# Kernel optimization log

Measured on AMD Instinct MI355X. Metric: run time of the kernel, lower is better.

Reference implementation:

```python
import jax, jax.numpy as jnp
import numpy as np

N_EMBD = 1024
N_HEAD = 16


def setup_inputs() -> dict:
    key = jax.random.key(0)
    ks = jax.random.split(key, 11)
    B, T, T2, C = 4, 2048, 1024, N_EMBD
    s = 0.02
    return {
        "x": jax.random.normal(ks[0], (B, T, C), jnp.float32),
        "enc_x": jax.random.normal(ks[1], (B, T2, C), jnp.float32),
        "Wq": jax.random.normal(ks[2], (C, C), jnp.float32) * s,
        "bq": jax.random.normal(ks[3], (C,), jnp.float32) * s,
        "Wk": jax.random.normal(ks[4], (C, C), jnp.float32) * s,
        "bk": jax.random.normal(ks[5], (C,), jnp.float32) * s,
        "Wv": jax.random.normal(ks[6], (C, C), jnp.float32) * s,
        "bv": jax.random.normal(ks[7], (C,), jnp.float32) * s,
        "Wo": jax.random.normal(ks[8], (C, C), jnp.float32) * s,
        "bo": jax.random.normal(ks[9], (C,), jnp.float32) * s,
    }


def reference(x, enc_x, Wq, bq, Wk, bk, Wv, bv, Wo, bo):
    B, T, C = x.shape
    B2, T2, C2 = enc_x.shape
    H = N_HEAD
    D = C // H  # head dim
    q = x @ Wq + bq          # [B,T,C]
    k = enc_x @ Wk + bk      # [B,T2,C]
    v = enc_x @ Wv + bv      # [B,T2,C]
    q = q.reshape(B, T, H, D).transpose(0, 2, 1, 3)    # [B,H,T,D]
    k = k.reshape(B2, T2, H, D).transpose(0, 2, 1, 3)  # [B,H,T2,D]
    v = v.reshape(B2, T2, H, D).transpose(0, 2, 1, 3)  # [B,H,T2,D]
    att = jnp.einsum("bhtd,bhsd->bhts", q, k) * (1.0 / jnp.sqrt(jnp.float32(D)))
    att = jax.nn.softmax(att, axis=-1)                 # [B,H,T,T2]
    y = jnp.einsum("bhts,bhsd->bhtd", att, v)          # [B,H,T,D]
    y = y.transpose(0, 2, 1, 3).reshape(B, T, C)
    return y @ Wo + bo
```

## Files before the change

### kernel.cpp

```cpp
#include <hip/hip_runtime.h>
#include <hip/hip_bf16.h>


typedef __bf16 bf16_t;
typedef __bf16 bf16x8 __attribute__((ext_vector_type(8)));
typedef float f32x4 __attribute__((ext_vector_type(4)));
typedef float f32x16 __attribute__((ext_vector_type(16)));
typedef unsigned int u32x4 __attribute__((ext_vector_type(4)));

#define AS1C(p) ((const __attribute__((address_space(1))) void*)(p))
#define AS3(p)  ((__attribute__((address_space(3))) void*)(p))

constexpr int CC  = 1024;
constexpr int TT  = 2048;
constexpr int TT2 = 1024;

#if __has_builtin(__builtin_amdgcn_exp2f)
__device__ __forceinline__ float EXP2(float x) { return __builtin_amdgcn_exp2f(x); }
#else
__device__ __forceinline__ float EXP2(float x) { return exp2f(x); }
#endif

__global__ __launch_bounds__(256) void prep(const float* __restrict__ x, bf16_t* __restrict__ xb,
                                            const float* __restrict__ enc, bf16_t* __restrict__ eb,
                                            const float* __restrict__ W0, const float* __restrict__ W1,
                                            const float* __restrict__ W2, const float* __restrict__ W3,
                                            bf16_t* __restrict__ T0, bf16_t* __restrict__ T1,
                                            bf16_t* __restrict__ T2, bf16_t* __restrict__ T3) {
    __shared__ float tile[32][33];
    const int bid = blockIdx.x;
    if (bid < 2048) {
        int t = bid * 256 + threadIdx.x;
        #pragma unroll
        for (int k = 0; k < 3; ++k) {
            int i = t + k * 524288;
            const float* in; bf16_t* out; int j;
            if (i < 1048576) { in = x;   out = xb; j = i; }
            else             { in = enc; out = eb; j = i - 1048576; }
            const float4* p = (const float4*)in + 2 * (size_t)j;
            float4 a = p[0], b = p[1];
            bf16x8 v;
            v[0] = (bf16_t)a.x; v[1] = (bf16_t)a.y; v[2] = (bf16_t)a.z; v[3] = (bf16_t)a.w;
            v[4] = (bf16_t)b.x; v[5] = (bf16_t)b.y; v[6] = (bf16_t)b.z; v[7] = (bf16_t)b.w;
            *(bf16x8*)(out + (size_t)j * 8) = v;
        }
    } else {
        int idx = bid - 2048;
        int bx = idx & 31, by = (idx >> 5) & 31, bz = idx >> 10;
        const float* W; bf16_t* Tt;
        switch (bz) {
            case 0:  W = W0; Tt = T0; break;
            case 1:  W = W1; Tt = T1; break;
            case 2:  W = W2; Tt = T2; break;
            default: W = W3; Tt = T3; break;
        }
        int xx = threadIdx.x & 31, yy = threadIdx.x >> 5;
        int bxe = bx * 32, bye = by * 32;
        for (int i = 0; i < 4; ++i) {
            int r = yy + i * 8;
            tile[r][xx] = W[(size_t)(bye + r) * 1024 + bxe + xx];
        }
        __syncthreads();
        for (int i = 0; i < 4; ++i) {
            int r = yy + i * 8;
            Tt[(size_t)(bxe + r) * 1024 + bye + xx] = (bf16_t)tile[xx][r];
        }
    }
}

#define SB0 __builtin_amdgcn_sched_barrier(0)
#define GLL(src, dst) __builtin_amdgcn_global_load_lds(AS1C(src), AS3(dst), 16, 0, 0)

__device__ __forceinline__ bf16x8 ldx(const char* p) { return *(const bf16x8*)p; }

__global__ __launch_bounds__(512, 2) void gemm_qkv8(const bf16_t* __restrict__ xb,
                                                    const bf16_t* __restrict__ eb,
                                                    const bf16_t* __restrict__ wtq,
                                                    const bf16_t* __restrict__ wtk,
                                                    const float* __restrict__ bq,
                                                    const float* __restrict__ bk,
                                                    const float* __restrict__ bv,
                                                    bf16_t* __restrict__ Qs,
                                                    bf16_t* __restrict__ Ks,
                                                    bf16_t* __restrict__ Vs,
                                                    float qscale) {
    __shared__ __align__(16) char GLDS[131072];
    char* ldsA = &GLDS[0];
    char* ldsB = &GLDS[65536];

    const int tid = threadIdx.x;
    const int w   = tid >> 6;
    const int l   = tid & 63;
    const int wm  = w >> 2;
    const int wn  = w & 3;
    const int l15 = l & 15, lhi = l >> 4;

    const int bid = blockIdx.x;
    const bf16_t* Ap; const bf16_t* Bp;
    int m0, n0;
    float scale;
    const float* bias; bf16_t* outp; int outn0;
    bool vout = false;
    if (bid < 128) {
        int xcd = bid & 7, j = bid >> 3;
        n0 = (j & 3) * 256; m0 = (xcd * 4 + (j >> 2)) * 256;
        Ap = xb; Bp = wtq; scale = qscale;
        bias = bq; outp = Qs; outn0 = n0;
    } else {
        int b2 = bid - 128;
        int xcd = b2 & 7, j = b2 >> 3;
        n0 = (j & 7) * 256; m0 = (xcd * 2 + (j >> 3)) * 256;
        Ap = eb; Bp = wtk; scale = 1.0f;
        if (n0 < 1024) { bias = bk; outp = Ks; outn0 = n0; }
        else           { bias = bv; outp = Vs; outn0 = n0 - 1024; vout = true; }
    }

    const int lrow  = l >> 3;
    const int lslot = (l & 7) ^ lrow;
    const char* Asrc = (const char*)(Ap + (size_t)(m0 + w * 16 + lrow) * 1024 + lslot * 8);
    const char* Bsrc = (const char*)(Bp + (size_t)(n0 + w * 16 + lrow) * 1024 + lslot * 8);
    #define STG_A(t, buf, h)                                                                   \
        do {                                                                                   \
            GLL(Asrc + (size_t)(h) * 262144 + (t) * 128,         ldsA + (buf) * 32768 + (h) * 16384 + w * 2048);        \
            GLL(Asrc + (size_t)(h) * 262144 + 16384 + (t) * 128, ldsA + (buf) * 32768 + (h) * 16384 + w * 2048 + 1024); \
        } while (0)
    #define STG_B(t, buf, h)                                                                   \
        do {                                                                                   \
            GLL(Bsrc + (size_t)(h) * 262144 + (t) * 128,         ldsB + (buf) * 32768 + (h) * 16384 + w * 2048);        \
            GLL(Bsrc + (size_t)(h) * 262144 + 16384 + (t) * 128, ldsB + (buf) * 32768 + (h) * 16384 + w * 2048 + 1024); \
        } while (0)

    const int aoff = (wm * 128 + l15) * 128;
    const int boff = (wn * 64 + l15) * 128;
    const int sl0  = ((0 + lhi) ^ (l15 & 7)) << 4;
    const int sl1  = ((4 + lhi) ^ (l15 & 7)) << 4;

    #define RD_A(dst, KA, qm)                                                    \
        do { _Pragma("unroll") for (int mf = 0; mf < 4; ++mf) {                  \
            dst[mf * 2 + 0] = ldx((KA) + aoff + ((qm) * 64 + mf * 16) * 128 + sl0); \
            dst[mf * 2 + 1] = ldx((KA) + aoff + ((qm) * 64 + mf * 16) * 128 + sl1); } } while (0)
    #define RD_B(dst, KB, qn)                                                    \
        do { _Pragma("unroll") for (int nf = 0; nf < 2; ++nf) {                  \
            dst[nf * 2 + 0] = ldx((KB) + boff + ((qn) * 32 + nf * 16) * 128 + sl0); \
            dst[nf * 2 + 1] = ldx((KB) + boff + ((qn) * 32 + nf * 16) * 128 + sl1); } } while (0)

    #define MFMA16(qm, qn, Af, Bf)                                                             \
        do { __builtin_amdgcn_s_setprio(1);                                                    \
            _Pragma("unroll") for (int mf = 0; mf < 4; ++mf)                                   \
            _Pragma("unroll") for (int nf = 0; nf < 2; ++nf) {                                 \
                acc[(qm) * 4 + mf][(qn) * 2 + nf] = __builtin_amdgcn_mfma_f32_16x16x32_bf16(   \
                    Af[mf * 2 + 0], Bf[nf * 2 + 0], acc[(qm) * 4 + mf][(qn) * 2 + nf], 0, 0, 0); \
                acc[(qm) * 4 + mf][(qn) * 2 + nf] = __builtin_amdgcn_mfma_f32_16x16x32_bf16(   \
                    Af[mf * 2 + 1], Bf[nf * 2 + 1], acc[(qm) * 4 + mf][(qn) * 2 + nf], 0, 0, 0); } \
            __builtin_amdgcn_s_setprio(0); } while (0)

    #define PH_BAR do { SB0; __builtin_amdgcn_s_barrier(); SB0;                                \
                        asm volatile("s_waitcnt lgkmcnt(0)" ::: "memory"); SB0; } while (0)
    #define PH_END do { SB0; __builtin_amdgcn_s_barrier(); SB0; } while (0)

    f32x4 acc[8][4] = {};
    bf16x8 A0[8], A1[8], B0[4], B1[4];

    STG_A(0, 0, 0); STG_A(0, 0, 1);
    STG_B(0, 0, 0); STG_B(0, 0, 1);
    STG_A(1, 1, 0); STG_A(1, 1, 1);
    asm volatile("s_waitcnt vmcnt(4)" ::: "memory");
    SB0; __builtin_amdgcn_s_barrier(); SB0;

    constexpr int NT = 16;
    for (int t = 0; t < NT; ++t) {
        const int buf = t & 1;
        const char* KA = ldsA + buf * 32768;
        const char* KB = ldsB + buf * 32768;

        if (t + 1 < NT) STG_B(t + 1, buf ^ 1, 0);
        RD_A(A0, KA, 0); RD_B(B0, KB, 0);
        PH_BAR;
        MFMA16(0, 0, A0, B0);
        PH_END;

        if (t + 1 < NT) STG_B(t + 1, buf ^ 1, 1);
        RD_A(A1, KA, 1);
        PH_BAR;
        MFMA16(1, 0, A1, B0);
        PH_END;

        if (t + 2 < NT) STG_A(t + 2, buf, 0);
        RD_B(B1, KB, 1);
        PH_BAR;
        MFMA16(1, 1, A1, B1);
        PH_END;

        if (t + 2 < NT) STG_A(t + 2, buf, 1);
        SB0; __builtin_amdgcn_s_barrier(); SB0;
        MFMA16(0, 1, A0, B1);
        if (t < NT - 2) asm volatile("s_waitcnt vmcnt(4)" ::: "memory");
        else            asm volatile("s_waitcnt vmcnt(0)" ::: "memory");
        PH_END;
    }

    __syncthreads();
    char* EP = GLDS + w * 16384;

    if (!vout) {
        #pragma unroll
        for (int ni = 0; ni < 4; ++ni) {
            int c_rel = ni * 16 + l15;
            float bvv = bias[outn0 + wn * 64 + c_rel];
            #pragma unroll
            for (int mi = 0; mi < 8; ++mi) {
                int mbase = mi * 16 + lhi * 4;
                #pragma unroll
                for (int r = 0; r < 4; ++r)
                    *(bf16_t*)(EP + (mbase + r) * 128 + c_rel * 2) =
                        (bf16_t)((acc[mi][ni][r] + bvv) * scale);
            }
        }
        asm volatile("s_waitcnt lgkmcnt(0)" ::: "memory");
        SB0;
        char* gbase = (char*)outp + (size_t)(m0 + wm * 128) * 2048 + (outn0 + wn * 64) * 2;
        #pragma unroll
        for (int i = 0; i < 16; ++i) {
            int m_rel = i * 8 + (l >> 3);
            int ch = l & 7;
            bf16x8 v = *(const bf16x8*)(EP + m_rel * 128 + ch * 16);
            *(bf16x8*)(gbase + (size_t)m_rel * 2048 + ch * 16) = v;
        }
    } else {
        int col0 = outn0 + wn * 64;
        int hh = col0 >> 6;
        int rowbase = m0 + wm * 128;
        int bb = rowbase >> 10, key0 = rowbase & 1023;
        #pragma unroll
        for (int ni = 0; ni < 4; ++ni) {
            int dd = ni * 16 + l15;
            float bvv = bias[col0 + dd];
            int sw = (dd & 7) << 4;
            #pragma unroll
            for (int mi = 0; mi < 8; ++mi) {
                int kb = mi * 16 + lhi * 4;
                #pragma unroll
                for (int r = 0; r < 4; ++r)
                    *(bf16_t*)(EP + dd * 256 + (((kb + r) * 2) ^ sw)) =
                        (bf16_t)((acc[mi][ni][r] + bvv) * scale);
            }
        }
        asm volatile("s_waitcnt lgkmcnt(0)" ::: "memory");
        SB0;
        char* gbase = (char*)outp + ((size_t)((bb * 16 + hh) * 64) * 1024 + key0) * 2;
        #pragma unroll
        for (int i = 0; i < 16; ++i) {
            int dd = i * 4 + (l >> 4);
            int ch = l & 15;
            bf16x8 v = *(const bf16x8*)(EP + dd * 256 + ((ch * 16) ^ ((dd & 7) << 4)));
            *(bf16x8*)(gbase + (size_t)dd * 2048 + ch * 16) = v;
        }
    }
    #undef STG_A
    #undef STG_B
    #undef RD_A
    #undef RD_B
    #undef MFMA16
    #undef PH_BAR
    #undef PH_END
}

__device__ __forceinline__ void gemm_body(bf16_t* As, bf16_t* Bs,
                                          const bf16_t* __restrict__ A,
                                          const bf16_t* __restrict__ Bt,
                                          const float* __restrict__ bias,
                                          float* __restrict__ out,
                                          int lgNT, int mband, int bid) {
    const int tid  = threadIdx.x;
    const int lane = tid & 63;
    const int wave = tid >> 6;
    const int wr = wave >> 1, wc = wave & 1;
    const int l15 = lane & 15, lhi = lane >> 4;

    const int xcd = bid & 7;
    const int j   = bid >> 3;
    const int n0  = (j & ((1 << lgNT) - 1)) * 128;
    const int m0  = (xcd * mband + (j >> lgNT)) * 128;

    f32x4 acc[4][4] = {};

    for (int k0 = 0; k0 < 1024; k0 += 32) {
        for (int i = 0; i < 2; ++i) {
            int e   = i * 2048 + wave * 512 + lane * 8;
            int row = e >> 5, col = e & 31;
            __builtin_amdgcn_global_load_lds(AS1C(A  + (size_t)(m0 + row) * 1024 + k0 + col),
                                             AS3(As + i * 2048 + wave * 512), 16, 0, 0);
            __builtin_amdgcn_global_load_lds(AS1C(Bt + (size_t)(n0 + row) * 1024 + k0 + col),
                                             AS3(Bs + i * 2048 + wave * 512), 16, 0, 0);
        }
        __syncthreads();
        bf16x8 a[4], b[4];
        #pragma unroll
        for (int m = 0; m < 4; ++m)
            a[m] = *(const bf16x8*)&As[(wr * 64 + m * 16 + l15) * 32 + lhi * 8];
        #pragma unroll
        for (int n = 0; n < 4; ++n)
            b[n] = *(const bf16x8*)&Bs[(wc * 64 + n * 16 + l15) * 32 + lhi * 8];
        #pragma unroll
        for (int m = 0; m < 4; ++m)
            #pragma unroll
            for (int n = 0; n < 4; ++n)
                acc[m][n] = __builtin_amdgcn_mfma_f32_16x16x32_bf16(a[m], b[n], acc[m][n], 0, 0, 0);
        __syncthreads();
    }

    #pragma unroll
    for (int n = 0; n < 4; ++n) {
        int col = n0 + wc * 64 + n * 16 + l15;
        float bv = bias[col];
        #pragma unroll
        for (int m = 0; m < 4; ++m) {
            int rowb = m0 + wr * 64 + m * 16 + lhi * 4;
            #pragma unroll
            for (int r = 0; r < 4; ++r)
                out[(size_t)(rowb + r) * 1024 + col] = acc[m][n][r] + bv;
        }
    }
}

__global__ __launch_bounds__(256) void gemm_out(const bf16_t* __restrict__ yb,
                                                const bf16_t* __restrict__ wto,
                                                const float* __restrict__ bo,
                                                float* __restrict__ out) {
    __shared__ __align__(16) bf16_t As[128 * 32];
    __shared__ __align__(16) bf16_t Bs[128 * 32];
    gemm_body(As, Bs, yb, wto, bo, out, 3, 8, blockIdx.x);
}

__device__ __forceinline__ unsigned pk_bf16(float lo, float hi) {
    unsigned r;
    asm("v_cvt_pk_bf16_f32 %0, %1, %2" : "=v"(r) : "v"(lo), "v"(hi));
    return r;
}
__device__ __forceinline__ void swap32(unsigned &a, unsigned &b) {
    asm("v_permlane32_swap_b32 %0, %1" : "+v"(a), "+v"(b));
}
__device__ __forceinline__ float sum_halves(float x) {
    unsigned a = __builtin_bit_cast(unsigned, x), b = a;
    swap32(a, b);
    return __builtin_bit_cast(float, a) + __builtin_bit_cast(float, b);
}
__device__ __forceinline__ bf16x8 ldsf(const bf16_t* base, int row, int colb) {
    int off = row * 128 + (colb ^ ((row & 7) << 4));
    return *(const bf16x8*)((const char*)base + off);
}
__device__ __forceinline__ bf16x8 packP(const f32x16& s0, const f32x16& s1, int kt) {
    const f32x16& sp = (kt < 2) ? s0 : s1;
    const int rb = (kt & 1) * 8;
    unsigned a0 = pk_bf16(sp[rb + 0], sp[rb + 1]);
    unsigned a1 = pk_bf16(sp[rb + 2], sp[rb + 3]);
    unsigned a2 = pk_bf16(sp[rb + 4], sp[rb + 5]);
    unsigned a3 = pk_bf16(sp[rb + 6], sp[rb + 7]);
    swap32(a0, a2);
    swap32(a1, a3);
    union { u32x4 u; bf16x8 h; } cv;
    cv.u = (u32x4){a0, a1, a2, a3};
    return cv.h;
}

__global__ __launch_bounds__(256, 2) void attn256(const bf16_t* __restrict__ Q,
                                                  const bf16_t* __restrict__ K,
                                                  const bf16_t* __restrict__ Vt,
                                                  bf16_t* __restrict__ Y) {
    __shared__ __align__(16) bf16_t SM[3][2][64 * 64];

    const int tid = threadIdx.x;
    const int l   = tid & 63;
    const int w   = tid >> 6;
    const int l31 = l & 31;
    const int lh  = l >> 5;

    const int bid = blockIdx.x;
    const int bh  = bid & 63;
    const int qb  = bid >> 6;
    const int b = bh >> 4, h = bh & 15;
    const int q0 = qb * 256 + w * 64;

    const bf16_t* Qb = Q + (size_t)b * TT * CC + h * 64;
    const char* Kc = (const char*)(K + (size_t)b * TT2 * CC + h * 64);
    const char* Vc = (const char*)(Vt + (size_t)bh * 64 * 1024);

    bf16x8 qfA[4], qfB[4];
    #pragma unroll
    for (int kt = 0; kt < 4; ++kt) {
        qfA[kt] = *(const bf16x8*)&Qb[(size_t)(q0 + l31)      * CC + kt * 16 + lh * 8];
        qfB[kt] = *(const bf16x8*)&Qb[(size_t)(q0 + 32 + l31) * CC + kt * 16 + lh * 8];
    }
    __builtin_amdgcn_sched_barrier(0);

    f32x16 yA0 = {}, yA1 = {}, yB0 = {}, yB1 = {};
    float lsA = 0.f, lsB = 0.f;

    const int krow = w * 16 + (l >> 3);
    const int ss   = ((l & 7) ^ (l >> 3)) & 7;
    const int off0 = krow * 2048 + ss * 16;
    const int off1 = off0 + 8 * 2048;

    #define STAGE(t, buf)                                                                 \
        do {                                                                              \
            __builtin_amdgcn_global_load_lds(AS1C(Kc + (size_t)(t) * 131072 + off0),      \
                                             AS3((char*)&SM[buf][0][0] + w * 2048), 16, 0, 0);        \
            __builtin_amdgcn_global_load_lds(AS1C(Kc + (size_t)(t) * 131072 + off1),      \
                                             AS3((char*)&SM[buf][0][0] + w * 2048 + 1024), 16, 0, 0); \
            __builtin_amdgcn_global_load_lds(AS1C(Vc + (t) * 128 + off0),                 \
                                             AS3((char*)&SM[buf][1][0] + w * 2048), 16, 0, 0);        \
            __builtin_amdgcn_global_load_lds(AS1C(Vc + (t) * 128 + off1),                 \
                                             AS3((char*)&SM[buf][1][0] + w * 2048 + 1024), 16, 0, 0); \
        } while (0)

    #define SUMEXP(s0, s1, ls)                                                    \
        do {                                                                      \
            float rs = 0.f;                                                       \
            _Pragma("unroll")                                                     \
            for (int r = 0; r < 16; ++r) {                                        \
                s0[r] = EXP2(s0[r]);                                              \
                s1[r] = EXP2(s1[r]);                                              \
                rs += s0[r] + s1[r];                                              \
            }                                                                     \
            ls += sum_halves(rs);                                                 \
        } while (0)

    constexpr int NT = TT2 / 64;
    STAGE(0, 0);
    STAGE(1, 1);

    int cur = 0;
    for (int t = 0; t < NT; ++t) {
        if (t + 1 < NT) asm volatile("s_waitcnt vmcnt(4)" ::: "memory");
        else            asm volatile("s_waitcnt vmcnt(0)" ::: "memory");
        __builtin_amdgcn_sched_barrier(0);
        __builtin_amdgcn_s_barrier();
        __builtin_amdgcn_sched_barrier(0);

        if (t + 2 < NT) {
            int nb = cur + 2; if (nb >= 3) nb -= 3;
            STAGE(t + 2, nb);
        }

        const bf16_t* Kl = &SM[cur][0][0];
        const bf16_t* Vl = &SM[cur][1][0];

        f32x16 sA0 = {}, sA1 = {}, sB0 = {}, sB1 = {};
        #pragma unroll
        for (int kt = 0; kt < 4; ++kt) {
            int colb = kt * 32 + (lh << 4);
            bf16x8 a0 = ldsf(Kl, l31,      colb);
            bf16x8 a1 = ldsf(Kl, 32 + l31, colb);
            sA0 = __builtin_amdgcn_mfma_f32_32x32x16_bf16(a0, qfA[kt], sA0, 0, 0, 0);
            sB0 = __builtin_amdgcn_mfma_f32_32x32x16_bf16(a0, qfB[kt], sB0, 0, 0, 0);
            sA1 = __builtin_amdgcn_mfma_f32_32x32x16_bf16(a1, qfA[kt], sA1, 0, 0, 0);
            sB1 = __builtin_amdgcn_mfma_f32_32x32x16_bf16(a1, qfB[kt], sB1, 0, 0, 0);
        }

        SUMEXP(sA0, sA1, lsA);
        SUMEXP(sB0, sB1, lsB);

        __builtin_amdgcn_s_setprio(1);
        #pragma unroll
        for (int kt = 0; kt < 4; ++kt) {
            bf16x8 pA = packP(sA0, sA1, kt);
            bf16x8 pB = packP(sB0, sB1, kt);
            int colb = kt * 32 + (lh << 4);
            bf16x8 v0 = ldsf(Vl, l31,      colb);
            bf16x8 v1 = ldsf(Vl, 32 + l31, colb);
            yA0 = __builtin_amdgcn_mfma_f32_32x32x16_bf16(v0, pA, yA0, 0, 0, 0);
            yA1 = __builtin_amdgcn_mfma_f32_32x32x16_bf16(v1, pA, yA1, 0, 0, 0);
            yB0 = __builtin_amdgcn_mfma_f32_32x32x16_bf16(v0, pB, yB0, 0, 0, 0);
            yB1 = __builtin_amdgcn_mfma_f32_32x32x16_bf16(v1, pB, yB1, 0, 0, 0);
        }
        __builtin_amdgcn_s_setprio(0);

        ++cur; if (cur == 3) cur = 0;
    }
    #undef STAGE
    #undef SUMEXP

    __syncthreads();

    float iA = 1.f / lsA, iB = 1.f / lsB;
    char* ob = (char*)&SM[0][0][0] + w * 8192;
    const int sw = (l31 & 7) << 4;
    #pragma unroll
    for (int r = 0; r < 16; ++r) {
        int drow = (r & 3) + 8 * (r >> 2) + 4 * lh;
        *(bf16_t*)(ob + l31 * 128 + ((drow * 2) ^ sw))               = (bf16_t)(yA0[r] * iA);
        *(bf16_t*)(ob + l31 * 128 + (((32 + drow) * 2) ^ sw))        = (bf16_t)(yA1[r] * iA);
        *(bf16_t*)(ob + 4096 + l31 * 128 + ((drow * 2) ^ sw))        = (bf16_t)(yB0[r] * iB);
        *(bf16_t*)(ob + 4096 + l31 * 128 + (((32 + drow) * 2) ^ sw)) = (bf16_t)(yB1[r] * iB);
    }
    __syncthreads();
    bf16_t* Yb = Y + (size_t)b * TT * CC + h * 64 + (size_t)q0 * CC;
    #pragma unroll
    for (int i = 0; i < 8; ++i) {
        int qr = i * 8 + (l >> 3);
        int c  = ((l & 7) * 16) ^ ((qr & 7) << 4);
        bf16x8 v = *(const bf16x8*)(ob + (qr >> 5) * 4096 + (qr & 31) * 128 + c);
        *(bf16x8*)&Yb[(size_t)qr * CC + (l & 7) * 8] = v;
    }
}

extern "C" void kernel_launch(void* const* d_in, const int* in_sizes, int n_in,
                              void* d_out, int out_size, void* d_ws, size_t ws_size,
                              hipStream_t stream) {
    const float* x   = (const float*)d_in[0];
    const float* enc = (const float*)d_in[1];
    const float* Wq  = (const float*)d_in[2];
    const float* bq  = (const float*)d_in[3];
    const float* Wk  = (const float*)d_in[4];
    const float* bk  = (const float*)d_in[5];
    const float* Wv  = (const float*)d_in[6];
    const float* bv  = (const float*)d_in[7];
    const float* Wo  = (const float*)d_in[8];
    const float* bo  = (const float*)d_in[9];

    char* w = (char*)d_ws;
    size_t o = 0;
    bf16_t* xb  = (bf16_t*)(w + o); o += (size_t)8192 * 1024 * 2;
    bf16_t* eb  = (bf16_t*)(w + o); o += (size_t)4096 * 1024 * 2;
    bf16_t* wtq = (bf16_t*)(w + o); o += (size_t)1024 * 1024 * 2;
    bf16_t* wtk = (bf16_t*)(w + o); o += (size_t)1024 * 1024 * 2;
    bf16_t* wtv = (bf16_t*)(w + o); o += (size_t)1024 * 1024 * 2;
    bf16_t* wto = (bf16_t*)(w + o); o += (size_t)1024 * 1024 * 2;
    bf16_t* Qs  = (bf16_t*)(w + o); o += (size_t)8192 * 1024 * 2;
    bf16_t* Ks  = (bf16_t*)(w + o); o += (size_t)4096 * 1024 * 2;
    bf16_t* Vt  = (bf16_t*)(w + o); o += (size_t)4096 * 1024 * 2;
    bf16_t* yb  = (bf16_t*)(w + o); o += (size_t)8192 * 1024 * 2;

    prep<<<6144, 256, 0, stream>>>(x, xb, enc, eb, Wq, Wk, Wv, Wo, wtq, wtk, wtv, wto);

    const float qscale = 0.125f * 1.4426950408889634f;
    gemm_qkv8<<<256, 512, 0, stream>>>(xb, eb, wtq, wtk, bq, bk, bv, Qs, Ks, Vt, qscale);

    attn256<<<512, 256, 0, stream>>>(Qs, Ks, Vt, yb);

    gemm_out<<<512, 256, 0, stream>>>(yb, wto, bo, (float*)d_out);
}
```

Baseline: 118.6 us.

## Load K tiles directly into registers and stage only V through LDS

```diff
diff --git a/kernel.cpp b/kernel.cpp
--- a/kernel.cpp
+++ b/kernel.cpp
@@ -345,9 +345,9 @@
     swap32(a, b);
     return __builtin_bit_cast(float, a) + __builtin_bit_cast(float, b);
 }
-__device__ __forceinline__ bf16x8 ldsf(const bf16_t* base, int row, int colb) {
+__device__ __forceinline__ bf16x8 ldsf(const char* base, int row, int colb) {
     int off = row * 128 + (colb ^ ((row & 7) << 4));
-    return *(const bf16x8*)((const char*)base + off);
+    return *(const bf16x8*)(base + off);
 }
 __device__ __forceinline__ bf16x8 packP(const f32x16& s0, const f32x16& s1, int kt) {
     const f32x16& sp = (kt < 2) ? s0 : s1;
@@ -363,11 +363,12 @@
     return cv.h;
 }
 
-__global__ __launch_bounds__(256, 2) void attn256(const bf16_t* __restrict__ Q,
-                                                  const bf16_t* __restrict__ K,
-                                                  const bf16_t* __restrict__ Vt,
-                                                  bf16_t* __restrict__ Y) {
-    __shared__ __align__(16) bf16_t SM[3][2][64 * 64];
+__global__ __launch_bounds__(256) __attribute__((amdgpu_waves_per_eu(2, 2)))
+void attn256(const bf16_t* __restrict__ Q,
+             const bf16_t* __restrict__ K,
+             const bf16_t* __restrict__ Vt,
+             bf16_t* __restrict__ Y) {
+    __shared__ __align__(16) char SMRAW[32768];
 
     const int tid = threadIdx.x;
     const int l   = tid & 63;
@@ -391,7 +392,7 @@
         qfA[kt] = *(const bf16x8*)&Qb[(size_t)(q0 + l31)      * CC + kt * 16 + lh * 8];
         qfB[kt] = *(const bf16x8*)&Qb[(size_t)(q0 + 32 + l31) * CC + kt * 16 + lh * 8];
     }
-    __builtin_amdgcn_sched_barrier(0);
+    SB0;
 
     f32x16 yA0 = {}, yA1 = {}, yB0 = {}, yB1 = {};
     float lsA = 0.f, lsB = 0.f;
@@ -401,17 +402,19 @@
     const int off0 = krow * 2048 + ss * 16;
     const int off1 = off0 + 8 * 2048;
 
-    #define STAGE(t, buf)                                                                 \
+    #define STAGEV(t, buf)                                                                \
         do {                                                                              \
-            __builtin_amdgcn_global_load_lds(AS1C(Kc + (size_t)(t) * 131072 + off0),      \
-                                             AS3((char*)&SM[buf][0][0] + w * 2048), 16, 0, 0);        \
-            __builtin_amdgcn_global_load_lds(AS1C(Kc + (size_t)(t) * 131072 + off1),      \
-                                             AS3((char*)&SM[buf][0][0] + w * 2048 + 1024), 16, 0, 0); \
             __builtin_amdgcn_global_load_lds(AS1C(Vc + (t) * 128 + off0),                 \
-                                             AS3((char*)&SM[buf][1][0] + w * 2048), 16, 0, 0);        \
+                                             AS3(SMRAW + (buf) * 8192 + w * 2048), 16, 0, 0);        \
             __builtin_amdgcn_global_load_lds(AS1C(Vc + (t) * 128 + off1),                 \
-                                             AS3((char*)&SM[buf][1][0] + w * 2048 + 1024), 16, 0, 0); \
+                                             AS3(SMRAW + (buf) * 8192 + w * 2048 + 1024), 16, 0, 0); \
         } while (0)
+
+    #define LDK(dst, t)                                                                   \
+        do { _Pragma("unroll") for (int kt = 0; kt < 4; ++kt) {                           \
+            dst[kt * 2 + 0] = *(const bf16x8*)(Kc + ((size_t)((t) * 64 + l31)      << 11) + kt * 32 + (lh << 4)); \
+            dst[kt * 2 + 1] = *(const bf16x8*)(Kc + ((size_t)((t) * 64 + 32 + l31) << 11) + kt * 32 + (lh << 4)); \
+        } } while (0)
 
     #define SUMEXP(s0, s1, ls)                                                    \
         do {                                                                      \
@@ -426,40 +429,42 @@
         } while (0)
 
     constexpr int NT = TT2 / 64;
-    STAGE(0, 0);
-    STAGE(1, 1);
+    bf16x8 kr[8];
+
+    STAGEV(0, 0);
+    STAGEV(1, 1);
+    SB0;
+    LDK(kr, 0);
+    SB0;
 
     int cur = 0;
     for (int t = 0; t < NT; ++t) {
-        if (t + 1 < NT) asm volatile("s_waitcnt vmcnt(4)" ::: "memory");
-        else            asm volatile("s_waitcnt vmcnt(0)" ::: "memory");
-        __builtin_amdgcn_sched_barrier(0);
+        asm volatile("s_waitcnt vmcnt(10)" ::: "memory");
+        SB0;
         __builtin_amdgcn_s_barrier();
-        __builtin_amdgcn_sched_barrier(0);
+        SB0;
+
+        f32x16 sA0 = {}, sA1 = {}, sB0 = {}, sB1 = {};
+        #pragma unroll
+        for (int kt = 0; kt < 4; ++kt) {
+            sA0 = __builtin_amdgcn_mfma_f32_32x32x16_bf16(kr[kt * 2 + 0], qfA[kt], sA0, 0, 0, 0);
+            sB0 = __builtin_amdgcn_mfma_f32_32x32x16_bf16(kr[kt * 2 + 0], qfB[kt], sB0, 0, 0, 0);
+            sA1 = __builtin_amdgcn_mfma_f32_32x32x16_bf16(kr[kt * 2 + 1], qfA[kt], sA1, 0, 0, 0);
+            sB1 = __builtin_amdgcn_mfma_f32_32x32x16_bf16(kr[kt * 2 + 1], qfB[kt], sB1, 0, 0, 0);
+        }
+        SB0;
 
         if (t + 2 < NT) {
             int nb = cur + 2; if (nb >= 3) nb -= 3;
-            STAGE(t + 2, nb);
-        }
-
-        const bf16_t* Kl = &SM[cur][0][0];
-        const bf16_t* Vl = &SM[cur][1][0];
-
-        f32x16 sA0 = {}, sA1 = {}, sB0 = {}, sB1 = {};
-        #pragma unroll
-        for (int kt = 0; kt < 4; ++kt) {
-            int colb = kt * 32 + (lh << 4);
-            bf16x8 a0 = ldsf(Kl, l31,      colb);
-            bf16x8 a1 = ldsf(Kl, 32 + l31, colb);
-            sA0 = __builtin_amdgcn_mfma_f32_32x32x16_bf16(a0, qfA[kt], sA0, 0, 0, 0);
-            sB0 = __builtin_amdgcn_mfma_f32_32x32x16_bf16(a0, qfB[kt], sB0, 0, 0, 0);
-            sA1 = __builtin_amdgcn_mfma_f32_32x32x16_bf16(a1, qfA[kt], sA1, 0, 0, 0);
-            sB1 = __builtin_amdgcn_mfma_f32_32x32x16_bf16(a1, qfB[kt], sB1, 0, 0, 0);
-        }
+            STAGEV(t + 2, nb);
+        }
+        if (t + 1 < NT) LDK(kr, t + 1);
+        SB0;
 
         SUMEXP(sA0, sA1, lsA);
         SUMEXP(sB0, sB1, lsB);
 
+        const char* Vl = SMRAW + cur * 8192;
         __builtin_amdgcn_s_setprio(1);
         #pragma unroll
         for (int kt = 0; kt < 4; ++kt) {
@@ -477,13 +482,14 @@
 
         ++cur; if (cur == 3) cur = 0;
     }
-    #undef STAGE
+    #undef STAGEV
+    #undef LDK
     #undef SUMEXP
 
     __syncthreads();
 
     float iA = 1.f / lsA, iB = 1.f / lsB;
-    char* ob = (char*)&SM[0][0][0] + w * 8192;
+    char* ob = SMRAW + w * 8192;
     const int sw = (l31 & 7) << 4;
     #pragma unroll
     for (int r = 0; r < 16; ++r) {
```

Measured after the change: 124.8 us. 1.05x slower.
